# Performance work log

Measured on AMD Instinct MI355X. Metric: run time of the kernel, lower is better.

The kernel has to match this reference:

```python
import jax, jax.numpy as jnp
import numpy as np

N, E = 50000, 800000
D, H, C, ED = 128, 8, 16, 4  # embed_dim, heads, head_dim, edge_dim


def _add_self_loops(edge_index, ea, n):
    # PyG add_self_loops with fill_value='mean': self-loop edge_attr is the
    # mean of incoming edge attributes per destination node (0 if none).
    src, dst = edge_index[0], edge_index[1]
    deg = jax.ops.segment_sum(jnp.ones((src.shape[0],), ea.dtype), dst, num_segments=n)
    loop_ea = jax.ops.segment_sum(ea, dst, num_segments=n) / jnp.maximum(deg, 1.0)[:, None]
    ar = jnp.arange(n, dtype=src.dtype)
    return (jnp.concatenate([src, ar]), jnp.concatenate([dst, ar]),
            jnp.concatenate([ea, loop_ea], axis=0))


def _gatv2(x, src, dst, ea, Wl, bl, Wr, br, We, att, bias, concat):
    n = x.shape[0]
    xl = (x @ Wl + bl).reshape(n, H, C)   # lin_l -> messages (source)
    xr = (x @ Wr + br).reshape(n, H, C)   # lin_r -> target
    e = (ea @ We).reshape(-1, H, C)       # lin_edge (no bias in PyG)
    m = jax.nn.leaky_relu(xl[src] + xr[dst] + e, negative_slope=0.2)  # [Etot,H,C]
    alpha = jnp.einsum('ehc,hc->eh', m, att)
    amax = jax.ops.segment_max(alpha, dst, num_segments=n)   # every node has a self loop
    ex = jnp.exp(alpha - amax[dst])
    den = jax.ops.segment_sum(ex, dst, num_segments=n)
    a = ex / den[dst]                                        # segment softmax over dst
    out = jax.ops.segment_sum(xl[src] * a[:, :, None], dst, num_segments=n)  # [N,H,C]
    out = out.reshape(n, H * C) if concat else out.mean(axis=1)
    return out + bias


def _ln(h, g, b):
    mu = h.mean(-1, keepdims=True)
    var = jnp.var(h, axis=-1, keepdims=True)
    return (h - mu) / jnp.sqrt(var + 1e-5) * g + b


def setup_inputs() -> dict:
    key = jax.random.key(0)
    ks = jax.random.split(key, 32)
    s = 0.05
    inp = {
        'x': jax.random.normal(ks[0], (N, D), jnp.float32),
        'edge_index': jax.random.randint(ks[1], (2, E), 0, N, jnp.int32),
        'edge_attr': jax.random.normal(ks[2], (E, ED), jnp.float32),
    }
    dims = [(D, H * C), (H * C, H * C), (H * C, C)]  # (in_dim, bias_dim per layer)
    k = 3
    for i, (din, bdim) in enumerate(dims):
        inp[f'Wl{i}'] = jax.random.normal(ks[k], (din, H * C), jnp.float32) * s; k += 1
        inp[f'bl{i}'] = jnp.zeros((H * C,), jnp.float32)
        inp[f'Wr{i}'] = jax.random.normal(ks[k], (din, H * C), jnp.float32) * s; k += 1
        inp[f'br{i}'] = jnp.zeros((H * C,), jnp.float32)
        inp[f'We{i}'] = jax.random.normal(ks[k], (ED, H * C), jnp.float32) * s; k += 1
        inp[f'att{i}'] = jax.random.normal(ks[k], (H, C), jnp.float32) * s; k += 1
        inp[f'b{i}'] = jnp.zeros((bdim,), jnp.float32)
        inp[f'g{i}'] = jnp.ones((bdim,), jnp.float32)
        inp[f'be{i}'] = jnp.zeros((bdim,), jnp.float32)
    inp['Wout'] = jax.random.normal(ks[k], (C, D), jnp.float32) * s
    inp['bout'] = jnp.zeros((D,), jnp.float32)
    return inp


def reference(x, edge_index, edge_attr,
              Wl0, bl0, Wr0, br0, We0, att0, b0, g0, be0,
              Wl1, bl1, Wr1, br1, We1, att1, b1, g1, be1,
              Wl2, bl2, Wr2, br2, We2, att2, b2, g2, be2,
              Wout, bout):
    n = x.shape[0]
    src, dst, ea = _add_self_loops(edge_index, edge_attr, n)
    layers = [
        (Wl0, bl0, Wr0, br0, We0, att0, b0, g0, be0, True),
        (Wl1, bl1, Wr1, br1, We1, att1, b1, g1, be1, True),
        (Wl2, bl2, Wr2, br2, We2, att2, b2, g2, be2, False),
    ]
    for (Wl, bl, Wr, br, We, att, bias, g, be, concat) in layers:
        h = _gatv2(x, src, dst, ea, Wl, bl, Wr, br, We, att, bias, concat)
        h = jax.nn.elu(h)
        h = _ln(h, g, be)
        if h.shape == x.shape:  # residual (layers 0,1)
            h = h + x
        x = h
    return x @ Wout + bout
```

## Files before the change

kernel.cpp:

```cpp
#include <hip/hip_runtime.h>
#include <hip/hip_bf16.h>

#define ND 128
#define NH 8
#define NC 16

typedef float v2f __attribute__((ext_vector_type(2)));

static inline size_t alignup(size_t x){ return (x + 255) & ~size_t(255); }

__device__ __forceinline__ ushort f2bf(float f){
    __hip_bfloat16 h = __float2bfloat16(f);
    return *reinterpret_cast<ushort*>(&h);
}

__device__ __forceinline__ v2f unpack_bf2(uint u){
    v2f r;
    r.x = __uint_as_float(u << 16);
    r.y = __uint_as_float(u & 0xffff0000u);
    return r;
}

__device__ __forceinline__ v2f lrelu2(v2f z){
    v2f s = z * 0.2f;
    v2f r;
    r.x = fmaxf(z.x, s.x);
    r.y = fmaxf(z.y, s.y);
    return r;
}

__device__ __forceinline__ float hred8(float x){
    int y;
    y = __builtin_amdgcn_mov_dpp(__float_as_int(x), 0xB1, 0xF, 0xF, true);
    x += __int_as_float(y);
    y = __builtin_amdgcn_mov_dpp(__float_as_int(x), 0x4E, 0xF, 0xF, true);
    x += __int_as_float(y);
    y = __builtin_amdgcn_mov_dpp(__float_as_int(x), 0x141, 0xF, 0xF, true);
    x += __int_as_float(y);
    return x;
}


__global__ void hist_kernel(const int* __restrict__ dsts, int* __restrict__ deg, int E)
{
    int e = blockIdx.x * blockDim.x + threadIdx.x;
    if (e >= E) return;
    atomicAdd(&deg[dsts[e]], 1);
}

__global__ __launch_bounds__(1024) void scan_kernel(const int* __restrict__ deg,
                                                    int* __restrict__ rowstart, int n)
{
    __shared__ int wsum[16];
    int tid = threadIdx.x;
    int lane = tid & 63, wid = tid >> 6;
    int carry = 0;
    for (int base = 0; base < n; base += 1024) {
        int idx = base + tid;
        int v = (idx < n) ? ((deg[idx] + 3) & ~3) : 0;
        int s = v;
        #pragma unroll
        for (int o = 1; o < 64; o <<= 1) {
            int t = __shfl_up(s, o);
            if (lane >= o) s += t;
        }
        if (lane == 63) wsum[wid] = s;
        __syncthreads();
        int off = 0;
        #pragma unroll
        for (int w = 0; w < 16; ++w) {
            int ws_ = wsum[w];
            if (w < wid) off += ws_;
        }
        int total = 0;
        #pragma unroll
        for (int w = 0; w < 16; ++w) total += wsum[w];
        if (idx < n) rowstart[idx] = carry + off + (s - v);
        carry += total;
        __syncthreads();
    }
    if (tid == 0) rowstart[n] = carry;
}

__global__ void scatter_kernel(const int* __restrict__ srcs, const int* __restrict__ dsts,
                               const float4* __restrict__ ea4,
                               const int* __restrict__ rowstart, int* __restrict__ cursor,
                               int* __restrict__ src_sorted, float4* __restrict__ ea_sorted, int E)
{
    int e = blockIdx.x * blockDim.x + threadIdx.x;
    if (e >= E) return;
    int d = dsts[e];
    int pos = rowstart[d] + atomicAdd(&cursor[d], 1);
    src_sorted[pos] = srcs[e];
    ea_sorted[pos] = ea4[e];
}

__global__ void padfill_kernel(const int* __restrict__ rowstart, const int* __restrict__ deg,
                               int* __restrict__ src_sorted, float4* __restrict__ ea_sorted, int n)
{
    int v = blockIdx.x * blockDim.x + threadIdx.x;
    if (v < n) {
        int d = deg[v];
        int p = rowstart[v] + d;
        int pe = rowstart[v] + ((d + 3) & ~3);
        for (; p < pe; ++p) {
            src_sorted[p] = 0;
            ea_sorted[p] = make_float4(0.f, 0.f, 0.f, 0.f);
        }
    } else if (v < n + 64) {
        int p = rowstart[n] + (v - n);
        src_sorted[p] = 0;
        ea_sorted[p] = make_float4(0.f, 0.f, 0.f, 0.f);
    }
}


__global__ __launch_bounds__(256) void gemm_xw2(const float* __restrict__ X,
                                                const float* __restrict__ Wl,
                                                const float* __restrict__ bl,
                                                const float* __restrict__ Wr,
                                                const float* __restrict__ br,
                                                ushort* __restrict__ XLB,
                                                float* __restrict__ XR, int nrows)
{
    __shared__ float xs[64][128];
    int tid = threadIdx.x;
    int row0 = blockIdx.x * 64;

    const float4* X4 = (const float4*)X;
    float4* xs4 = (float4*)xs;
    #pragma unroll
    for (int i = tid; i < 64*32; i += 256) {
        int r = i >> 5;
        float4 v = make_float4(0.f, 0.f, 0.f, 0.f);
        if (row0 + r < nrows) v = X4[(size_t)(row0 + r) * 32 + (i & 31)];
        xs4[i] = v;
    }
    __syncthreads();

    int cg = tid & 31;
    int rg = (tid >> 5) * 8;
    float accl[8][4], accr[8][4];
    float4 blv = ((const float4*)bl)[cg];
    float4 brv = ((const float4*)br)[cg];
    #pragma unroll
    for (int r = 0; r < 8; r++) {
        accl[r][0] = blv.x; accl[r][1] = blv.y; accl[r][2] = blv.z; accl[r][3] = blv.w;
        accr[r][0] = brv.x; accr[r][1] = brv.y; accr[r][2] = brv.z; accr[r][3] = brv.w;
    }

    #pragma unroll 2
    for (int k = 0; k < 128; k++) {
        float4 wl = ((const float4*)(Wl + (size_t)k * 128))[cg];
        float4 wr = ((const float4*)(Wr + (size_t)k * 128))[cg];
        #pragma unroll
        for (int r = 0; r < 8; r++) {
            float xv = xs[rg + r][k];
            accl[r][0] = fmaf(xv, wl.x, accl[r][0]);
            accl[r][1] = fmaf(xv, wl.y, accl[r][1]);
            accl[r][2] = fmaf(xv, wl.z, accl[r][2]);
            accl[r][3] = fmaf(xv, wl.w, accl[r][3]);
            accr[r][0] = fmaf(xv, wr.x, accr[r][0]);
            accr[r][1] = fmaf(xv, wr.y, accr[r][1]);
            accr[r][2] = fmaf(xv, wr.z, accr[r][2]);
            accr[r][3] = fmaf(xv, wr.w, accr[r][3]);
        }
    }

    #pragma unroll
    for (int r = 0; r < 8; r++) {
        int row = row0 + rg + r;
        if (row < nrows) {
            ushort4 ob;
            ob.x = f2bf(accl[r][0]); ob.y = f2bf(accl[r][1]);
            ob.z = f2bf(accl[r][2]); ob.w = f2bf(accl[r][3]);
            ((ushort4*)XLB)[(size_t)row * 32 + cg] = ob;
            float4 of = make_float4(accr[r][0], accr[r][1], accr[r][2], accr[r][3]);
            ((float4*)XR)[(size_t)row * 32 + cg] = of;
        }
    }
}


__device__ __forceinline__ void gat_wave(
    int dstv, int t,
    const uint* __restrict__ xl_u, const float* __restrict__ xr,
    const int* __restrict__ rowstart, const int* __restrict__ deg,
    const int* __restrict__ src_sorted, const float4* __restrict__ ea_sorted,
    const float* __restrict__ We, const float* __restrict__ att,
    v2f& r_out, float& l_out)
{
    v2f xrv  = ((const v2f*)(xr + (size_t)dstv * ND))[t];
    v2f we0  = ((const v2f*)(We))[t];
    v2f we1  = ((const v2f*)(We + ND))[t];
    v2f we2  = ((const v2f*)(We + 2*ND))[t];
    v2f we3  = ((const v2f*)(We + 3*ND))[t];
    v2f attv = ((const v2f*)att)[t];

    int p0 = __builtin_amdgcn_readfirstlane(rowstart[dstv]);
    int dv = __builtin_amdgcn_readfirstlane(deg[dstv]);
    int pads = (dv + 3) & ~3;

    uint xsw = xl_u[(((uint)dstv) << 6) + t];

    const int* sp = src_sorted + p0;
    const float4* ep = ea_sorted + p0;

    v2f s01 = {0.f, 0.f}, s23 = {0.f, 0.f};
    v2f a = {0.f, 0.f};
    float lsum = 0.f;

    int4 sA = *(const int4*)(sp);
    uint xA0 = xl_u[(((uint)sA.x) << 6) + t];
    uint xA1 = xl_u[(((uint)sA.y) << 6) + t];
    uint xA2 = xl_u[(((uint)sA.z) << 6) + t];
    uint xA3 = xl_u[(((uint)sA.w) << 6) + t];
    int4 sB = *(const int4*)(sp + 4);
    uint xB0 = xl_u[(((uint)sB.x) << 6) + t];
    uint xB1 = xl_u[(((uint)sB.y) << 6) + t];
    uint xB2 = xl_u[(((uint)sB.z) << 6) + t];
    uint xB3 = xl_u[(((uint)sB.w) << 6) + t];
    int4 sC = *(const int4*)(sp + 8);

    for (int p = 0; p < pads; p += 4) {
        uint xC0 = xl_u[(((uint)sC.x) << 6) + t];
        uint xC1 = xl_u[(((uint)sC.y) << 6) + t];
        uint xC2 = xl_u[(((uint)sC.z) << 6) + t];
        uint xC3 = xl_u[(((uint)sC.w) << 6) + t];
        int4 sD = *(const int4*)(sp + p + 12);
        float4 ea0 = ep[p];
        float4 ea1 = ep[p + 1];
        float4 ea2 = ep[p + 2];
        float4 ea3 = ep[p + 3];

        v2f b0 = xrv + we0*ea0.x + we1*ea0.y + we2*ea0.z + we3*ea0.w;
        v2f b1 = xrv + we0*ea1.x + we1*ea1.y + we2*ea1.z + we3*ea1.w;
        v2f b2 = xrv + we0*ea2.x + we1*ea2.y + we2*ea2.z + we3*ea2.w;
        v2f b3 = xrv + we0*ea3.x + we1*ea3.y + we2*ea3.z + we3*ea3.w;

        s01 += (v2f){ea0.x, ea0.y}; s23 += (v2f){ea0.z, ea0.w};
        s01 += (v2f){ea1.x, ea1.y}; s23 += (v2f){ea1.z, ea1.w};
        s01 += (v2f){ea2.x, ea2.y}; s23 += (v2f){ea2.z, ea2.w};
        s01 += (v2f){ea3.x, ea3.y}; s23 += (v2f){ea3.z, ea3.w};

        v2f x0 = unpack_bf2(xA0);
        v2f x1 = unpack_bf2(xA1);
        v2f x2 = unpack_bf2(xA2);
        v2f x3 = unpack_bf2(xA3);

        v2f l0 = lrelu2(x0 + b0);
        v2f l1 = lrelu2(x1 + b1);
        v2f l2 = lrelu2(x2 + b2);
        v2f l3 = lrelu2(x3 + b3);

        v2f q0 = l0 * attv;
        v2f q1 = l1 * attv;
        v2f q2 = l2 * attv;
        v2f q3 = l3 * attv;
        float pt0 = q0.x + q0.y;
        float pt1 = q1.x + q1.y;
        float pt2 = q2.x + q2.y;
        float pt3 = q3.x + q3.y;

        int live = dv - p;
        pt1 = (live > 1) ? pt1 : -1e30f;
        pt2 = (live > 2) ? pt2 : -1e30f;
        pt3 = (live > 3) ? pt3 : -1e30f;

        float al0 = hred8(pt0);
        float al1 = hred8(pt1);
        float al2 = hred8(pt2);
        float al3 = hred8(pt3);

        float pe0 = __expf(al0);
        float pe1 = __expf(al1);
        float pe2 = __expf(al2);
        float pe3 = __expf(al3);
        lsum += (pe0 + pe1) + (pe2 + pe3);
        a += x0 * pe0;
        a += x1 * pe1;
        a += x2 * pe2;
        a += x3 * pe3;

        xA0 = xB0; xA1 = xB1; xA2 = xB2; xA3 = xB3;
        xB0 = xC0; xB1 = xC1; xB2 = xC2; xB3 = xC3;
        sC = sD;
    }

    float inv = 1.0f / (float)(dv > 0 ? dv : 1);
    s01 *= inv; s23 *= inv;
    v2f xs = unpack_bf2(xsw);
    v2f bs = xrv + we0*s01.x + we1*s01.y + we2*s23.x + we3*s23.y;
    v2f ls = lrelu2(xs + bs);
    v2f qs = ls * attv;
    float al = hred8(qs.x + qs.y);
    float pe = __expf(al);
    l_out = lsum + pe;
    r_out = a + xs * pe;
}

__global__ __launch_bounds__(256) void attn_concat(
    const ushort* __restrict__ xlb, const float* __restrict__ xr,
    const float* __restrict__ xin,
    const int* __restrict__ rowstart, const int* __restrict__ deg,
    const int* __restrict__ src_sorted, const float4* __restrict__ ea_sorted,
    const float* __restrict__ We, const float* __restrict__ att,
    const float* __restrict__ bias, const float* __restrict__ g, const float* __restrict__ be,
    float* __restrict__ out, int n)
{
    int wid = threadIdx.x >> 6;
    int t = threadIdx.x & 63;
    int dstv = blockIdx.x * 4 + wid;
    if (dstv >= n) return;

    v2f av; float l;
    gat_wave(dstv, t, (const uint*)xlb, xr, rowstart, deg, src_sorted, ea_sorted, We, att, av, l);

    v2f bv = ((const v2f*)bias)[t];
    float linv = 1.0f / l;
    v2f h = av * linv + bv;
    h.x = h.x > 0.f ? h.x : (__expf(h.x) - 1.0f);
    h.y = h.y > 0.f ? h.y : (__expf(h.y) - 1.0f);

    float ss = h.x + h.y, qq = h.x*h.x + h.y*h.y;
    #pragma unroll
    for (int o = 1; o < 64; o <<= 1) { ss += __shfl_xor(ss, o); qq += __shfl_xor(qq, o); }
    float mu = ss * (1.0f / ND);
    float var = qq * (1.0f / ND) - mu * mu;
    float rstd = rsqrtf(var + 1e-5f);

    v2f gv  = ((const v2f*)g)[t];
    v2f bev = ((const v2f*)be)[t];
    v2f xiv = ((const v2f*)(xin + (size_t)dstv * ND))[t];
    v2f o2 = (h - mu) * rstd * gv + bev + xiv;
    ((v2f*)(out + (size_t)dstv * ND))[t] = o2;
}

__global__ __launch_bounds__(256) void attn_final(
    const ushort* __restrict__ xlb, const float* __restrict__ xr,
    const int* __restrict__ rowstart, const int* __restrict__ deg,
    const int* __restrict__ src_sorted, const float4* __restrict__ ea_sorted,
    const float* __restrict__ We, const float* __restrict__ att,
    const float* __restrict__ b2, const float* __restrict__ g2, const float* __restrict__ be2,
    const float* __restrict__ Wout, const float* __restrict__ bout,
    float* __restrict__ out, int n)
{
    __shared__ float h16s[4][16];
    int wid = threadIdx.x >> 6;
    int t = threadIdx.x & 63;
    int dstv = blockIdx.x * 4 + wid;
    if (dstv >= n) return;

    v2f av; float l;
    gat_wave(dstv, t, (const uint*)xlb, xr, rowstart, deg, src_sorted, ea_sorted, We, att, av, l);
    float linv = 1.0f / l;
    float v0 = av.x * linv, v1 = av.y * linv;

    #pragma unroll
    for (int o = 8; o < 64; o <<= 1) { v0 += __shfl_xor(v0, o); v1 += __shfl_xor(v1, o); }
    int cc = t & 7;
    float2 b2v = ((const float2*)b2)[cc];
    v0 = v0 * (1.0f / NH) + b2v.x;
    v1 = v1 * (1.0f / NH) + b2v.y;
    v0 = v0 > 0.f ? v0 : (__expf(v0) - 1.0f);
    v1 = v1 > 0.f ? v1 : (__expf(v1) - 1.0f);

    float ss = v0 + v1, qq = v0*v0 + v1*v1;
    #pragma unroll
    for (int o = 1; o < 8; o <<= 1) { ss += __shfl_xor(ss, o); qq += __shfl_xor(qq, o); }
    float mu = ss * (1.0f / NC);
    float var = qq * (1.0f / NC) - mu * mu;
    float rstd = rsqrtf(var + 1e-5f);
    float2 g2v = ((const float2*)g2)[cc];
    float2 be2v = ((const float2*)be2)[cc];
    float t0 = (v0 - mu) * rstd * g2v.x + be2v.x;
    float t1 = (v1 - mu) * rstd * g2v.y + be2v.y;

    if (t < 8) { h16s[wid][2*t] = t0; h16s[wid][2*t + 1] = t1; }

    float2 ov = ((const float2*)bout)[t];
    #pragma unroll
    for (int k = 0; k < NC; k++) {
        float hk = h16s[wid][k];
        float2 wv = ((const float2*)Wout)[k * 64 + t];
        ov.x = fmaf(hk, wv.x, ov.x);
        ov.y = fmaf(hk, wv.y, ov.y);
    }
    ((float2*)(out + (size_t)dstv * ND))[t] = ov;
}


extern "C" void kernel_launch(void* const* d_in, const int* in_sizes, int n_in,
                              void* d_out, int out_size, void* d_ws, size_t ws_size,
                              hipStream_t stream)
{
    const float* x_in = (const float*)d_in[0];
    const int*   ei   = (const int*)d_in[1];
    const float* ea   = (const float*)d_in[2];
    const int N = in_sizes[0] / ND;
    const int E = in_sizes[1] / 2;
    const int* srcs = ei;
    const int* dsts = ei + E;
    const float4* ea4 = (const float4*)ea;

    const float *Wl[3], *bl[3], *Wr[3], *br[3], *We[3], *att[3], *bb[3], *gg[3], *be[3];
    for (int l = 0; l < 3; l++) {
        int b = 3 + 9 * l;
        Wl[l]  = (const float*)d_in[b + 0];
        bl[l]  = (const float*)d_in[b + 1];
        Wr[l]  = (const float*)d_in[b + 2];
        br[l]  = (const float*)d_in[b + 3];
        We[l]  = (const float*)d_in[b + 4];
        att[l] = (const float*)d_in[b + 5];
        bb[l]  = (const float*)d_in[b + 6];
        gg[l]  = (const float*)d_in[b + 7];
        be[l]  = (const float*)d_in[b + 8];
    }
    const float* Wout = (const float*)d_in[30];
    const float* bout = (const float*)d_in[31];

    const size_t EP = (size_t)E + 3 * (size_t)N + 80;

    char* ws = (char*)d_ws;
    size_t off = 0;
    int* deg        = (int*)(ws + off);      off = alignup(off + (size_t)N * 4);
    int* cursor     = (int*)(ws + off);      off = alignup(off + (size_t)N * 4);
    size_t zero_bytes = off;
    int* rowstart   = (int*)(ws + off);      off = alignup(off + (size_t)(N + 1) * 4);
    int* src_sorted = (int*)(ws + off);      off = alignup(off + EP * 4);
    float4* ea_sorted = (float4*)(ws + off); off = alignup(off + EP * 16);
    ushort* xlb     = (ushort*)(ws + off);   off = alignup(off + (size_t)N * ND * 2);
    float* xr       = (float*)(ws + off);    off = alignup(off + (size_t)N * ND * 4);
    float* xa       = (float*)(ws + off);    off = alignup(off + (size_t)N * ND * 4);
    float* xb       = (float*)d_out;

    hipMemsetAsync(d_ws, 0, zero_bytes, stream);

    int ethreads = 256;
    int eblocks = (E + ethreads - 1) / ethreads;
    hist_kernel<<<eblocks, ethreads, 0, stream>>>(dsts, deg, E);
    scan_kernel<<<1, 1024, 0, stream>>>(deg, rowstart, N);
    padfill_kernel<<<(N + 64 + 255) / 256, 256, 0, stream>>>(rowstart, deg, src_sorted, ea_sorted, N);
    scatter_kernel<<<eblocks, ethreads, 0, stream>>>(srcs, dsts, ea4, rowstart, cursor,
                                                     src_sorted, ea_sorted, E);

    int gblocks = (N + 63) / 64;
    int ablocks = (N + 3) / 4;

    gemm_xw2<<<gblocks, 256, 0, stream>>>(x_in, Wl[0], bl[0], Wr[0], br[0], xlb, xr, N);
    attn_concat<<<ablocks, 256, 0, stream>>>(xlb, xr, x_in, rowstart, deg, src_sorted, ea_sorted,
                                             We[0], att[0], bb[0], gg[0], be[0], xa, N);
    gemm_xw2<<<gblocks, 256, 0, stream>>>(xa, Wl[1], bl[1], Wr[1], br[1], xlb, xr, N);
    attn_concat<<<ablocks, 256, 0, stream>>>(xlb, xr, xa, rowstart, deg, src_sorted, ea_sorted,
                                             We[1], att[1], bb[1], gg[1], be[1], xb, N);
    gemm_xw2<<<gblocks, 256, 0, stream>>>(xb, Wl[2], bl[2], Wr[2], br[2], xlb, xr, N);
    attn_final<<<ablocks, 256, 0, stream>>>(xlb, xr, rowstart, deg, src_sorted, ea_sorted,
                                            We[2], att[2], bb[2], gg[2], be[2],
                                            Wout, bout, (float*)d_out, N);
}
```

Baseline: 474.9 us.

## Store xr in bf16, precompute self-loop edge means, pre-shift source indices, use exp2

Several micro-optimizations land at once. xr is now stored as bf16, halving its write and read traffic. The self-loop mean edge attribute is computed once in a new easum kernel rather than re-accumulated in every attention layer. Source indices are pre-shifted by 8 (byte offsets) to drop address arithmetic, and the live-edge masking runs only on the last block. The exp is replaced by exp2 with the attention vector pre-scaled by log2(e), and the GEMM uses packed v2f FMAs. Together these trim bandwidth and ALU work in the attention kernels, at the cost of extra bf16 rounding on xr.

```diff
diff --git a/kernel.cpp b/kernel.cpp
--- a/kernel.cpp
+++ b/kernel.cpp
@@ -85,18 +85,18 @@
 __global__ void scatter_kernel(const int* __restrict__ srcs, const int* __restrict__ dsts,
                                const float4* __restrict__ ea4,
                                const int* __restrict__ rowstart, int* __restrict__ cursor,
-                               int* __restrict__ src_sorted, float4* __restrict__ ea_sorted, int E)
+                               int* __restrict__ srcb_sorted, float4* __restrict__ ea_sorted, int E)
 {
     int e = blockIdx.x * blockDim.x + threadIdx.x;
     if (e >= E) return;
     int d = dsts[e];
     int pos = rowstart[d] + atomicAdd(&cursor[d], 1);
-    src_sorted[pos] = srcs[e];
+    srcb_sorted[pos] = srcs[e] << 8;
     ea_sorted[pos] = ea4[e];
 }
 
 __global__ void padfill_kernel(const int* __restrict__ rowstart, const int* __restrict__ deg,
-                               int* __restrict__ src_sorted, float4* __restrict__ ea_sorted, int n)
+                               int* __restrict__ srcb_sorted, float4* __restrict__ ea_sorted, int n)
 {
     int v = blockIdx.x * blockDim.x + threadIdx.x;
     if (v < n) {
@@ -104,14 +104,29 @@
         int p = rowstart[v] + d;
         int pe = rowstart[v] + ((d + 3) & ~3);
         for (; p < pe; ++p) {
-            src_sorted[p] = 0;
+            srcb_sorted[p] = 0;
             ea_sorted[p] = make_float4(0.f, 0.f, 0.f, 0.f);
         }
     } else if (v < n + 64) {
         int p = rowstart[n] + (v - n);
-        src_sorted[p] = 0;
+        srcb_sorted[p] = 0;
         ea_sorted[p] = make_float4(0.f, 0.f, 0.f, 0.f);
     }
+}
+
+__global__ void easum_kernel(const int* __restrict__ rowstart, const int* __restrict__ deg,
+                             const float4* __restrict__ ea_sorted, float4* __restrict__ easum, int n)
+{
+    int v = blockIdx.x * blockDim.x + threadIdx.x;
+    if (v >= n) return;
+    int p0 = rowstart[v], d = deg[v];
+    float sx = 0.f, sy = 0.f, sz = 0.f, sw = 0.f;
+    for (int p = p0; p < p0 + d; ++p) {
+        float4 a = ea_sorted[p];
+        sx += a.x; sy += a.y; sz += a.z; sw += a.w;
+    }
+    float inv = 1.0f / (float)(d > 0 ? d : 1);
+    easum[v] = make_float4(sx * inv, sy * inv, sz * inv, sw * inv);
 }
 
 
@@ -121,7 +136,7 @@
                                                 const float* __restrict__ Wr,
                                                 const float* __restrict__ br,
                                                 ushort* __restrict__ XLB,
-                                                float* __restrict__ XR, int nrows)
+                                                ushort* __restrict__ XRB, int nrows)
 {
     __shared__ float xs[64][128];
     int tid = threadIdx.x;
@@ -140,30 +155,29 @@
 
     int cg = tid & 31;
     int rg = (tid >> 5) * 8;
-    float accl[8][4], accr[8][4];
+    v2f al0[8], al1[8], ar0[8], ar1[8];
     float4 blv = ((const float4*)bl)[cg];
     float4 brv = ((const float4*)br)[cg];
     #pragma unroll
     for (int r = 0; r < 8; r++) {
-        accl[r][0] = blv.x; accl[r][1] = blv.y; accl[r][2] = blv.z; accl[r][3] = blv.w;
-        accr[r][0] = brv.x; accr[r][1] = brv.y; accr[r][2] = brv.z; accr[r][3] = brv.w;
+        al0[r] = (v2f){blv.x, blv.y}; al1[r] = (v2f){blv.z, blv.w};
+        ar0[r] = (v2f){brv.x, brv.y}; ar1[r] = (v2f){brv.z, brv.w};
     }
 
     #pragma unroll 2
     for (int k = 0; k < 128; k++) {
         float4 wl = ((const float4*)(Wl + (size_t)k * 128))[cg];
         float4 wr = ((const float4*)(Wr + (size_t)k * 128))[cg];
+        v2f wl01 = (v2f){wl.x, wl.y}, wl23 = (v2f){wl.z, wl.w};
+        v2f wr01 = (v2f){wr.x, wr.y}, wr23 = (v2f){wr.z, wr.w};
         #pragma unroll
         for (int r = 0; r < 8; r++) {
             float xv = xs[rg + r][k];
-            accl[r][0] = fmaf(xv, wl.x, accl[r][0]);
-            accl[r][1] = fmaf(xv, wl.y, accl[r][1]);
-            accl[r][2] = fmaf(xv, wl.z, accl[r][2]);
-            accl[r][3] = fmaf(xv, wl.w, accl[r][3]);
-            accr[r][0] = fmaf(xv, wr.x, accr[r][0]);
-            accr[r][1] = fmaf(xv, wr.y, accr[r][1]);
-            accr[r][2] = fmaf(xv, wr.z, accr[r][2]);
-            accr[r][3] = fmaf(xv, wr.w, accr[r][3]);
+            v2f xv2 = (v2f){xv, xv};
+            al0[r] += xv2 * wl01;
+            al1[r] += xv2 * wl23;
+            ar0[r] += xv2 * wr01;
+            ar1[r] += xv2 * wr23;
         }
     }
 
@@ -171,12 +185,13 @@
     for (int r = 0; r < 8; r++) {
         int row = row0 + rg + r;
         if (row < nrows) {
-            ushort4 ob;
-            ob.x = f2bf(accl[r][0]); ob.y = f2bf(accl[r][1]);
-            ob.z = f2bf(accl[r][2]); ob.w = f2bf(accl[r][3]);
-            ((ushort4*)XLB)[(size_t)row * 32 + cg] = ob;
-            float4 of = make_float4(accr[r][0], accr[r][1], accr[r][2], accr[r][3]);
-            ((float4*)XR)[(size_t)row * 32 + cg] = of;
+            ushort4 ol, orr;
+            ol.x = f2bf(al0[r].x); ol.y = f2bf(al0[r].y);
+            ol.z = f2bf(al1[r].x); ol.w = f2bf(al1[r].y);
+            orr.x = f2bf(ar0[r].x); orr.y = f2bf(ar0[r].y);
+            orr.z = f2bf(ar1[r].x); orr.w = f2bf(ar1[r].y);
+            ((ushort4*)XLB)[(size_t)row * 32 + cg] = ol;
+            ((ushort4*)XRB)[(size_t)row * 32 + cg] = orr;
         }
     }
 }
@@ -184,64 +199,61 @@
 
 __device__ __forceinline__ void gat_wave(
     int dstv, int t,
-    const uint* __restrict__ xl_u, const float* __restrict__ xr,
+    const uint* __restrict__ xl_u, const uint* __restrict__ xr_u,
     const int* __restrict__ rowstart, const int* __restrict__ deg,
-    const int* __restrict__ src_sorted, const float4* __restrict__ ea_sorted,
+    const int* __restrict__ srcb_sorted, const float4* __restrict__ ea_sorted,
+    const float4* __restrict__ easum,
     const float* __restrict__ We, const float* __restrict__ att,
     v2f& r_out, float& l_out)
 {
-    v2f xrv  = ((const v2f*)(xr + (size_t)dstv * ND))[t];
     v2f we0  = ((const v2f*)(We))[t];
     v2f we1  = ((const v2f*)(We + ND))[t];
     v2f we2  = ((const v2f*)(We + 2*ND))[t];
     v2f we3  = ((const v2f*)(We + 3*ND))[t];
-    v2f attv = ((const v2f*)att)[t];
+    v2f attv = ((const v2f*)att)[t] * 1.44269504f;
+    v2f xrv  = unpack_bf2(xr_u[(((uint)dstv) << 6) + t]);
 
     int p0 = __builtin_amdgcn_readfirstlane(rowstart[dstv]);
     int dv = __builtin_amdgcn_readfirstlane(deg[dstv]);
-    int pads = (dv + 3) & ~3;
+    int nb = (dv + 3) >> 2;
 
     uint xsw = xl_u[(((uint)dstv) << 6) + t];
 
-    const int* sp = src_sorted + p0;
+    const int* sp = srcb_sorted + p0;
     const float4* ep = ea_sorted + p0;
-
-    v2f s01 = {0.f, 0.f}, s23 = {0.f, 0.f};
+    const char* xlc = (const char*)xl_u;
+    uint t4 = (uint)t * 4u;
+
     v2f a = {0.f, 0.f};
     float lsum = 0.f;
 
     int4 sA = *(const int4*)(sp);
-    uint xA0 = xl_u[(((uint)sA.x) << 6) + t];
-    uint xA1 = xl_u[(((uint)sA.y) << 6) + t];
-    uint xA2 = xl_u[(((uint)sA.z) << 6) + t];
-    uint xA3 = xl_u[(((uint)sA.w) << 6) + t];
+    uint xA0 = *(const uint*)(xlc + ((uint)sA.x + t4));
+    uint xA1 = *(const uint*)(xlc + ((uint)sA.y + t4));
+    uint xA2 = *(const uint*)(xlc + ((uint)sA.z + t4));
+    uint xA3 = *(const uint*)(xlc + ((uint)sA.w + t4));
     int4 sB = *(const int4*)(sp + 4);
-    uint xB0 = xl_u[(((uint)sB.x) << 6) + t];
-    uint xB1 = xl_u[(((uint)sB.y) << 6) + t];
-    uint xB2 = xl_u[(((uint)sB.z) << 6) + t];
-    uint xB3 = xl_u[(((uint)sB.w) << 6) + t];
+    uint xB0 = *(const uint*)(xlc + ((uint)sB.x + t4));
+    uint xB1 = *(const uint*)(xlc + ((uint)sB.y + t4));
+    uint xB2 = *(const uint*)(xlc + ((uint)sB.z + t4));
+    uint xB3 = *(const uint*)(xlc + ((uint)sB.w + t4));
     int4 sC = *(const int4*)(sp + 8);
 
-    for (int p = 0; p < pads; p += 4) {
-        uint xC0 = xl_u[(((uint)sC.x) << 6) + t];
-        uint xC1 = xl_u[(((uint)sC.y) << 6) + t];
-        uint xC2 = xl_u[(((uint)sC.z) << 6) + t];
-        uint xC3 = xl_u[(((uint)sC.w) << 6) + t];
-        int4 sD = *(const int4*)(sp + p + 12);
-        float4 ea0 = ep[p];
-        float4 ea1 = ep[p + 1];
-        float4 ea2 = ep[p + 2];
-        float4 ea3 = ep[p + 3];
+    for (int ib = 0; ib < nb; ++ib) {
+        uint xC0 = *(const uint*)(xlc + ((uint)sC.x + t4));
+        uint xC1 = *(const uint*)(xlc + ((uint)sC.y + t4));
+        uint xC2 = *(const uint*)(xlc + ((uint)sC.z + t4));
+        uint xC3 = *(const uint*)(xlc + ((uint)sC.w + t4));
+        int4 sD = *(const int4*)(sp + ib*4 + 12);
+        float4 ea0 = ep[ib*4];
+        float4 ea1 = ep[ib*4 + 1];
+        float4 ea2 = ep[ib*4 + 2];
+        float4 ea3 = ep[ib*4 + 3];
 
         v2f b0 = xrv + we0*ea0.x + we1*ea0.y + we2*ea0.z + we3*ea0.w;
         v2f b1 = xrv + we0*ea1.x + we1*ea1.y + we2*ea1.z + we3*ea1.w;
         v2f b2 = xrv + we0*ea2.x + we1*ea2.y + we2*ea2.z + we3*ea2.w;
         v2f b3 = xrv + we0*ea3.x + we1*ea3.y + we2*ea3.z + we3*ea3.w;
-
-        s01 += (v2f){ea0.x, ea0.y}; s23 += (v2f){ea0.z, ea0.w};
-        s01 += (v2f){ea1.x, ea1.y}; s23 += (v2f){ea1.z, ea1.w};
-        s01 += (v2f){ea2.x, ea2.y}; s23 += (v2f){ea2.z, ea2.w};
-        s01 += (v2f){ea3.x, ea3.y}; s23 += (v2f){ea3.z, ea3.w};
 
         v2f x0 = unpack_bf2(xA0);
         v2f x1 = unpack_bf2(xA1);
@@ -262,20 +274,22 @@
         float pt2 = q2.x + q2.y;
         float pt3 = q3.x + q3.y;
 
-        int live = dv - p;
-        pt1 = (live > 1) ? pt1 : -1e30f;
-        pt2 = (live > 2) ? pt2 : -1e30f;
-        pt3 = (live > 3) ? pt3 : -1e30f;
+        if (ib == nb - 1) {
+            int live = dv - ib*4;
+            pt1 = (live > 1) ? pt1 : -1e30f;
+            pt2 = (live > 2) ? pt2 : -1e30f;
+            pt3 = (live > 3) ? pt3 : -1e30f;
+        }
 
         float al0 = hred8(pt0);
         float al1 = hred8(pt1);
         float al2 = hred8(pt2);
         float al3 = hred8(pt3);
 
-        float pe0 = __expf(al0);
-        float pe1 = __expf(al1);
-        float pe2 = __expf(al2);
-        float pe3 = __expf(al3);
+        float pe0 = exp2f(al0);
+        float pe1 = exp2f(al1);
+        float pe2 = exp2f(al2);
+        float pe3 = exp2f(al3);
         lsum += (pe0 + pe1) + (pe2 + pe3);
         a += x0 * pe0;
         a += x1 * pe1;
@@ -287,23 +301,23 @@
         sC = sD;
     }
 
-    float inv = 1.0f / (float)(dv > 0 ? dv : 1);
-    s01 *= inv; s23 *= inv;
+    float4 em = easum[dstv];
     v2f xs = unpack_bf2(xsw);
-    v2f bs = xrv + we0*s01.x + we1*s01.y + we2*s23.x + we3*s23.y;
+    v2f bs = xrv + we0*em.x + we1*em.y + we2*em.z + we3*em.w;
     v2f ls = lrelu2(xs + bs);
     v2f qs = ls * attv;
     float al = hred8(qs.x + qs.y);
-    float pe = __expf(al);
+    float pe = exp2f(al);
     l_out = lsum + pe;
     r_out = a + xs * pe;
 }
 
 __global__ __launch_bounds__(256) void attn_concat(
-    const ushort* __restrict__ xlb, const float* __restrict__ xr,
+    const ushort* __restrict__ xlb, const ushort* __restrict__ xrb,
     const float* __restrict__ xin,
     const int* __restrict__ rowstart, const int* __restrict__ deg,
-    const int* __restrict__ src_sorted, const float4* __restrict__ ea_sorted,
+    const int* __restrict__ srcb_sorted, const float4* __restrict__ ea_sorted,
+    const float4* __restrict__ easum,
     const float* __restrict__ We, const float* __restrict__ att,
     const float* __restrict__ bias, const float* __restrict__ g, const float* __restrict__ be,
     float* __restrict__ out, int n)
@@ -314,7 +328,8 @@
     if (dstv >= n) return;
 
     v2f av; float l;
-    gat_wave(dstv, t, (const uint*)xlb, xr, rowstart, deg, src_sorted, ea_sorted, We, att, av, l);
+    gat_wave(dstv, t, (const uint*)xlb, (const uint*)xrb, rowstart, deg, srcb_sorted,
+             ea_sorted, easum, We, att, av, l);
 
     v2f bv = ((const v2f*)bias)[t];
     float linv = 1.0f / l;
@@ -337,9 +352,10 @@
 }
 
 __global__ __launch_bounds__(256) void attn_final(
-    const ushort* __restrict__ xlb, const float* __restrict__ xr,
+    const ushort* __restrict__ xlb, const ushort* __restrict__ xrb,
     const int* __restrict__ rowstart, const int* __restrict__ deg,
-    const int* __restrict__ src_sorted, const float4* __restrict__ ea_sorted,
+    const int* __restrict__ srcb_sorted, const float4* __restrict__ ea_sorted,
+    const float4* __restrict__ easum,
     const float* __restrict__ We, const float* __restrict__ att,
     const float* __restrict__ b2, const float* __restrict__ g2, const float* __restrict__ be2,
     const float* __restrict__ Wout, const float* __restrict__ bout,
@@ -352,7 +368,8 @@
     if (dstv >= n) return;
 
     v2f av; float l;
-    gat_wave(dstv, t, (const uint*)xlb, xr, rowstart, deg, src_sorted, ea_sorted, We, att, av, l);
+    gat_wave(dstv, t, (const uint*)xlb, (const uint*)xrb, rowstart, deg, srcb_sorted,
+             ea_sorted, easum, We, att, av, l);
     float linv = 1.0f / l;
     float v0 = av.x * linv, v1 = av.y * linv;
 
@@ -427,10 +444,11 @@
     int* cursor     = (int*)(ws + off);      off = alignup(off + (size_t)N * 4);
     size_t zero_bytes = off;
     int* rowstart   = (int*)(ws + off);      off = alignup(off + (size_t)(N + 1) * 4);
-    int* src_sorted = (int*)(ws + off);      off = alignup(off + EP * 4);
+    int* srcb_sorted = (int*)(ws + off);     off = alignup(off + EP * 4);
     float4* ea_sorted = (float4*)(ws + off); off = alignup(off + EP * 16);
+    float4* easum   = (float4*)(ws + off);   off = alignup(off + (size_t)N * 16);
     ushort* xlb     = (ushort*)(ws + off);   off = alignup(off + (size_t)N * ND * 2);
-    float* xr       = (float*)(ws + off);    off = alignup(off + (size_t)N * ND * 4);
+    ushort* xrb     = (ushort*)(ws + off);   off = alignup(off + (size_t)N * ND * 2);
     float* xa       = (float*)(ws + off);    off = alignup(off + (size_t)N * ND * 4);
     float* xb       = (float*)d_out;
 
@@ -440,21 +458,22 @@
     int eblocks = (E + ethreads - 1) / ethreads;
     hist_kernel<<<eblocks, ethreads, 0, stream>>>(dsts, deg, E);
     scan_kernel<<<1, 1024, 0, stream>>>(deg, rowstart, N);
-    padfill_kernel<<<(N + 64 + 255) / 256, 256, 0, stream>>>(rowstart, deg, src_sorted, ea_sorted, N);
+    padfill_kernel<<<(N + 64 + 255) / 256, 256, 0, stream>>>(rowstart, deg, srcb_sorted, ea_sorted, N);
     scatter_kernel<<<eblocks, ethreads, 0, stream>>>(srcs, dsts, ea4, rowstart, cursor,
-                                                     src_sorted, ea_sorted, E);
+                                                     srcb_sorted, ea_sorted, E);
+    easum_kernel<<<(N + 255) / 256, 256, 0, stream>>>(rowstart, deg, ea_sorted, easum, N);
 
     int gblocks = (N + 63) / 64;
     int ablocks = (N + 3) / 4;
 
-    gemm_xw2<<<gblocks, 256, 0, stream>>>(x_in, Wl[0], bl[0], Wr[0], br[0], xlb, xr, N);
-    attn_concat<<<ablocks, 256, 0, stream>>>(xlb, xr, x_in, rowstart, deg, src_sorted, ea_sorted,
-                                             We[0], att[0], bb[0], gg[0], be[0], xa, N);
-    gemm_xw2<<<gblocks, 256, 0, stream>>>(xa, Wl[1], bl[1], Wr[1], br[1], xlb, xr, N);
-    attn_concat<<<ablocks, 256, 0, stream>>>(xlb, xr, xa, rowstart, deg, src_sorted, ea_sorted,
-                                             We[1], att[1], bb[1], gg[1], be[1], xb, N);
-    gemm_xw2<<<gblocks, 256, 0, stream>>>(xb, Wl[2], bl[2], Wr[2], br[2], xlb, xr, N);
-    attn_final<<<ablocks, 256, 0, stream>>>(xlb, xr, rowstart, deg, src_sorted, ea_sorted,
-                                            We[2], att[2], bb[2], gg[2], be[2],
+    gemm_xw2<<<gblocks, 256, 0, stream>>>(x_in, Wl[0], bl[0], Wr[0], br[0], xlb, xrb, N);
+    attn_concat<<<ablocks, 256, 0, stream>>>(xlb, xrb, x_in, rowstart, deg, srcb_sorted, ea_sorted,
+                                             easum, We[0], att[0], bb[0], gg[0], be[0], xa, N);
+    gemm_xw2<<<gblocks, 256, 0, stream>>>(xa, Wl[1], bl[1], Wr[1], br[1], xlb, xrb, N);
+    attn_concat<<<ablocks, 256, 0, stream>>>(xlb, xrb, xa, rowstart, deg, srcb_sorted, ea_sorted,
+                                             easum, We[1], att[1], bb[1], gg[1], be[1], xb, N);
+    gemm_xw2<<<gblocks, 256, 0, stream>>>(xb, Wl[2], bl[2], Wr[2], br[2], xlb, xrb, N);
+    attn_final<<<ablocks, 256, 0, stream>>>(xlb, xrb, rowstart, deg, srcb_sorted, ea_sorted,
+                                            easum, We[2], att[2], bb[2], gg[2], be[2],
                                             Wout, bout, (float*)d_out, N);
 }
```

Measured after the change: 480.5 us. No clear change (+1.2%).
